# Kernel tuning notes

Measured on AMD Instinct MI355X. Metric: run time of the kernel, lower is better.

The kernel has to match this reference:

```python
import jax, jax.numpy as jnp
import numpy as np

N_NODES = 50000
N_EDGES = 1600000
E_DIM = 128
N_LAYERS = 3
N_GRAPHS = 32


def setup_inputs() -> dict:
    key = jax.random.key(0)
    ks = jax.random.split(key, 12)
    x = jax.random.normal(ks[0], (N_NODES,), dtype=jnp.float32)
    edge_index = jax.random.randint(ks[1], (2, N_EDGES), 0, N_NODES, dtype=jnp.int32)
    batch = jnp.sort(jax.random.randint(ks[2], (N_NODES,), 0, N_GRAPHS, dtype=jnp.int32))
    s_in = 1.0  # fan_in = 1 for the first linear
    s_e = 1.0 / np.sqrt(E_DIM)
    lin_w = jax.random.normal(ks[3], (1, E_DIM), jnp.float32) * s_in
    lin_b = jax.random.normal(ks[4], (E_DIM,), jnp.float32) * 0.01
    gcn_w = jax.random.normal(ks[5], (N_LAYERS, E_DIM, E_DIM), jnp.float32) * s_e
    gcn_b = jax.random.normal(ks[6], (N_LAYERS, E_DIM), jnp.float32) * 0.01
    r1_w = jax.random.normal(ks[7], (E_DIM, E_DIM), jnp.float32) * s_e
    r1_b = jax.random.normal(ks[8], (E_DIM,), jnp.float32) * 0.01
    r2_w = jax.random.normal(ks[9], (E_DIM, 1), jnp.float32) * s_e
    r2_b = jax.random.normal(ks[10], (1,), jnp.float32) * 0.01
    return {"x": x, "edge_index": edge_index, "batch": batch,
            "lin_w": lin_w, "lin_b": lin_b, "gcn_w": gcn_w, "gcn_b": gcn_b,
            "r1_w": r1_w, "r1_b": r1_b, "r2_w": r2_w, "r2_b": r2_b}


def reference(x, edge_index, batch, lin_w, lin_b, gcn_w, gcn_b, r1_w, r1_b, r2_w, r2_b):
    # input embedding: x.view(-1, 1) @ W + b -> [N, E]
    h = x.reshape(-1, 1) @ lin_w + lin_b

    # GCN normalization (add self-loops, symmetric deg^-1/2 norm) — structure is
    # identical across layers, so compute once.
    loops = jnp.arange(N_NODES, dtype=edge_index.dtype)
    src = jnp.concatenate([edge_index[0], loops])
    dst = jnp.concatenate([edge_index[1], loops])
    deg = jax.ops.segment_sum(jnp.ones(src.shape[0], h.dtype), dst, num_segments=N_NODES)
    dinv = jnp.where(deg > 0, jax.lax.rsqrt(deg), 0.0)
    norm = (dinv[src] * dinv[dst])[:, None]  # [E+N, 1]

    # NOTE: original calls x.relu() without assignment -> no activation (faithful).
    for l in range(N_LAYERS):
        h = h @ gcn_w[l]                                        # [N, E]
        h = jax.ops.segment_sum(h[src] * norm, dst, num_segments=N_NODES) + gcn_b[l]

    # global_add_pool over graphs
    pooled = jax.ops.segment_sum(h, batch, num_segments=N_GRAPHS)  # [G, E]
    hr = jnp.tanh(pooled @ r1_w + r1_b)
    return hr @ r2_w + r2_b  # [G, 1]
```

## Files before the change

### kernel.cpp

```cpp
#include <hip/hip_runtime.h>
#include <math.h>

#define NGRAPH 32
#define CAP 10240
#define EPT 16
#define EPB (256 * EPT)
#define BLK 256

__device__ __forceinline__ int block_scan_excl(int v, int tid, int* wsum, int& total) {
    int x = v;
#pragma unroll
    for (int d = 1; d < 64; d <<= 1) {
        int t = __shfl_up(x, d);
        if ((tid & 63) >= d) x += t;
    }
    if ((tid & 63) == 63) wsum[tid >> 6] = x;
    __syncthreads();
    if (tid == 0) {
        int a = 0;
#pragma unroll
        for (int i = 0; i < 4; i++) { int t = wsum[i]; wsum[i] = a; a += t; }
        wsum[4] = a;
    }
    __syncthreads();
    total = wsum[4];
    return x - v + wsum[tid >> 6];
}

__global__ __launch_bounds__(256, 4) void k_part(
        const int* __restrict__ src, const int* __restrict__ dst,
        int* __restrict__ gcursor, unsigned int* __restrict__ packed, int E) {
    __shared__ unsigned int ldsbuf[EPB];
    __shared__ int hist[256], lofs[256], lcur[256], base[256], wsum[5];
    int tid = threadIdx.x;
    int e0 = blockIdx.x * EPB;
    hist[tid] = 0;
    __syncthreads();
    int d_[EPT], s_[EPT];
#pragma unroll
    for (int c = 0; c < EPT / 4; c++) {
        int e = e0 + c * 1024 + (tid << 2);
        if (e + 3 < E) {
            int4 dv = *(const int4*)&dst[e];
            int4 sv = *(const int4*)&src[e];
            d_[4*c+0] = dv.x; d_[4*c+1] = dv.y; d_[4*c+2] = dv.z; d_[4*c+3] = dv.w;
            s_[4*c+0] = sv.x; s_[4*c+1] = sv.y; s_[4*c+2] = sv.z; s_[4*c+3] = sv.w;
            atomicAdd(&hist[dv.x >> 8], 1);
            atomicAdd(&hist[dv.y >> 8], 1);
            atomicAdd(&hist[dv.z >> 8], 1);
            atomicAdd(&hist[dv.w >> 8], 1);
        } else {
#pragma unroll
            for (int k = 0; k < 4; k++) {
                int ee = e + k;
                if (ee < E) {
                    d_[4*c+k] = dst[ee]; s_[4*c+k] = src[ee];
                    atomicAdd(&hist[d_[4*c+k] >> 8], 1);
                } else {
                    d_[4*c+k] = -1;
                }
            }
        }
    }
    __syncthreads();
    int v = hist[tid];
    int total;
    int excl = block_scan_excl(v, tid, wsum, total);
    lofs[tid] = excl;
    lcur[tid] = excl;
    if (v > 0) base[tid] = tid * CAP + atomicAdd(&gcursor[tid], v);
    __syncthreads();
#pragma unroll
    for (int c = 0; c < EPT; c++) {
        int dd = d_[c];
        if (dd >= 0) {
            int bk = dd >> 8;
            int slot = atomicAdd(&lcur[bk], 1);
            ldsbuf[slot] = ((unsigned int)bk << 24) | ((unsigned int)s_[c] << 8)
                         | (unsigned int)(dd & 255);
        }
    }
    __syncthreads();
    for (int i = tid; i < total; i += BLK) {
        unsigned int w = ldsbuf[i];
        int bk = w >> 24;
        packed[base[bk] + (i - lofs[bk])] = w & 0xFFFFFFu;
    }
}

__global__ __launch_bounds__(256) void k_bucket_chain(
        const unsigned int* __restrict__ packed, const int* __restrict__ gcursor,
        const float* __restrict__ x, const int* __restrict__ batch,
        int2* __restrict__ meta, float2* __restrict__ q0,
        float2* __restrict__ q1, float2* __restrict__ q2,
        unsigned short* __restrict__ csr, float* __restrict__ S, int N, int NB,
        const float* __restrict__ lin_w, const float* __restrict__ lin_b,
        const float* __restrict__ gcn_w, const float* __restrict__ gcn_b,
        float* __restrict__ chainv) {
    __shared__ union {
        struct {
            unsigned int buf[CAP];
            __align__(16) unsigned short lcsr[CAP];
            int cnt[256], lcur[256], wsum[5];
            float cs[NGRAPH];
        } b;
        struct { float v4[512]; } c;
    } sm;
    int tid = threadIdx.x;
    int b = blockIdx.x;

    if (b == NB) {
        float* v4 = sm.c.v4;
        int j = tid & 127, gg = tid >> 7;
        if (tid < 128) {
            v4[tid]       = lin_w[tid];
            v4[128 + tid] = lin_b[tid];
            v4[256 + tid] = gcn_b[tid];
            v4[384 + tid] = gcn_b[128 + tid];
        }
        __syncthreads();
        for (int l = 0; l < 3; l++) {
            const float* W = gcn_w + l * 128 * 128;
            float a0 = 0.f, a1 = 0.f;
            for (int k0 = 0; k0 < 128; k0 += 16) {
                float wreg[16];
#pragma unroll
                for (int t = 0; t < 16; t++) wreg[t] = W[(k0 + t) * 128 + j];
#pragma unroll
                for (int t = 0; t < 16; t++) {
                    a0 += v4[gg * 128 + k0 + t] * wreg[t];
                    a1 += v4[(gg + 2) * 128 + k0 + t] * wreg[t];
                }
            }
            __syncthreads();
            v4[gg * 128 + j] = a0;
            bool upd = (gg == 0) ? (l >= 1) : (l >= 2);
            if (upd) v4[(gg + 2) * 128 + j] = a1;
            __syncthreads();
        }
        chainv[tid]       = v4[tid];
        chainv[256 + tid] = v4[256 + tid];
        return;
    }

    int start = b * CAP;
    int len = gcursor[b];
    sm.b.cnt[tid] = 0;
    if (tid < NGRAPH) sm.b.cs[tid] = 0.f;
    __syncthreads();
    for (int e = tid; e < len; e += BLK) {
        unsigned int w = packed[start + e];
        sm.b.buf[e] = w;
        atomicAdd(&sm.b.cnt[w & 255], 1);
    }
    __syncthreads();
    int v = sm.b.cnt[tid];
    int vp = (v + 3) & ~3;
    int total;
    int excl = block_scan_excl(vp, tid, sm.b.wsum, total);
    sm.b.lcur[tid] = excl;
    int node = b * 256 + tid;
    if (node < N) {
        meta[node] = make_int2(start + excl, v);
        float dv = rsqrtf((float)(v + 1));
        q0[node] = make_float2(x[node] * dv, dv);
        atomicAdd(&sm.b.cs[batch[node]], 1.f);
        for (int p = v; p < vp; p++)
            sm.b.lcsr[excl + p] = (unsigned short)N;
    }
    if (b == 0 && tid == 0) {
        q0[N] = make_float2(0.f, 0.f);
        q1[N] = make_float2(0.f, 0.f);
        q2[N] = make_float2(0.f, 0.f);
    }
    __syncthreads();
    for (int e = tid; e < len; e += BLK) {
        unsigned int w = sm.b.buf[e];
        sm.b.lcsr[atomicAdd(&sm.b.lcur[w & 255], 1)] = (unsigned short)(w >> 8);
    }
    if (tid < NGRAPH && sm.b.cs[tid] != 0.f) atomicAdd(&S[tid], sm.b.cs[tid]);
    __syncthreads();
    const uint2* ls = (const uint2*)sm.b.lcsr;
    uint2* gs = (uint2*)&csr[start];
    for (int i = tid; i < (total >> 2); i += BLK) gs[i] = ls[i];
}

__global__ __launch_bounds__(256) void k_hop1(
        const float2* __restrict__ qin, float2* __restrict__ outv,
        const unsigned short* __restrict__ csr,
        const int2* __restrict__ meta, int N) {
    int tid  = threadIdx.x;
    int lane = tid & 7;
    int node = blockIdx.x * 32 + (tid >> 3);
    if (node >= N) return;
    int2 md = meta[node];
    int e = md.x, ne = md.y;
    float sx = 0.0f, su = 0.0f;
    for (int j = 4 * lane; j < ne; j += 32) {
        ushort4 c = *(const ushort4*)&csr[e + j];
        float2 a0 = qin[c.x], a1 = qin[c.y], a2 = qin[c.z], a3 = qin[c.w];
        sx += (a0.x + a1.x) + (a2.x + a3.x);
        su += (a0.y + a1.y) + (a2.y + a3.y);
    }
#pragma unroll
    for (int m = 4; m > 0; m >>= 1) {
        sx += __shfl_xor(sx, m);
        su += __shfl_xor(su, m);
    }
    if (lane == 0) {
        float2 qs = qin[node];
        float dv = rsqrtf((float)(ne + 1));
        float px = dv * (sx + qs.x), pu = dv * (su + qs.y);
        outv[node] = make_float2(px * dv, pu * dv);
    }
}

__global__ __launch_bounds__(256) void k_hop2(
        const float2* __restrict__ qin, float2* __restrict__ outv,
        const unsigned short* __restrict__ csr,
        const int2* __restrict__ meta, const int* __restrict__ batch,
        float* __restrict__ gp1, int N, int NBLK) {
    __shared__ float aS[NGRAPH];
    int tid  = threadIdx.x;
    int lane = tid & 7;
    int node = blockIdx.x * 32 + (tid >> 3);
    if (tid < NGRAPH) aS[tid] = 0.f;
    __syncthreads();
    if (node < N) {
        int2 md = meta[node];
        int e = md.x, ne = md.y;
        float sx = 0.0f, su = 0.0f;
        for (int j = 4 * lane; j < ne; j += 32) {
            ushort4 c = *(const ushort4*)&csr[e + j];
            float2 a0 = qin[c.x], a1 = qin[c.y], a2 = qin[c.z], a3 = qin[c.w];
            sx += (a0.x + a1.x) + (a2.x + a3.x);
            su += (a0.y + a1.y) + (a2.y + a3.y);
        }
#pragma unroll
        for (int m = 4; m > 0; m >>= 1) {
            sx += __shfl_xor(sx, m);
            su += __shfl_xor(su, m);
        }
        if (lane == 0) {
            float2 qs = qin[node];
            float dv = rsqrtf((float)(ne + 1));
            float px = dv * (sx + qs.x), pu = dv * (su + qs.y);
            outv[node] = make_float2(px * dv, pu * dv);
            atomicAdd(&aS[batch[node]], qs.y * sqrtf((float)(ne + 1)));
        }
    }
    __syncthreads();
    if (tid < NGRAPH) gp1[tid * NBLK + blockIdx.x] = aS[tid];
}

__global__ __launch_bounds__(256) void k_hop3(
        const float2* __restrict__ qin,
        const unsigned short* __restrict__ csr,
        const int2* __restrict__ meta, const int* __restrict__ batch,
        float* __restrict__ gp2, float* __restrict__ gp3, float* __restrict__ gp4,
        int N, int NBLK) {
    __shared__ float aS[NGRAPH], aV[NGRAPH], aU[NGRAPH];
    int tid  = threadIdx.x;
    int lane = tid & 7;
    int node = blockIdx.x * 32 + (tid >> 3);
    if (tid < NGRAPH) { aS[tid] = 0.f; aV[tid] = 0.f; aU[tid] = 0.f; }
    __syncthreads();
    if (node < N) {
        int2 md = meta[node];
        int e = md.x, ne = md.y;
        float sx = 0.0f, su = 0.0f;
        for (int j = 4 * lane; j < ne; j += 32) {
            ushort4 c = *(const ushort4*)&csr[e + j];
            float2 a0 = qin[c.x], a1 = qin[c.y], a2 = qin[c.z], a3 = qin[c.w];
            sx += (a0.x + a1.x) + (a2.x + a3.x);
            su += (a0.y + a1.y) + (a2.y + a3.y);
        }
#pragma unroll
        for (int m = 4; m > 0; m >>= 1) {
            sx += __shfl_xor(sx, m);
            su += __shfl_xor(su, m);
        }
        if (lane == 0) {
            float2 qs = qin[node];
            float dv = rsqrtf((float)(ne + 1));
            float px = dv * (sx + qs.x), pu = dv * (su + qs.y);
            int g = batch[node];
            atomicAdd(&aS[g], qs.y * sqrtf((float)(ne + 1)));
            atomicAdd(&aV[g], px);
            atomicAdd(&aU[g], pu);
        }
    }
    __syncthreads();
    if (tid < NGRAPH) {
        int slot = tid * NBLK + blockIdx.x;
        gp2[slot] = aS[tid];
        gp3[slot] = aV[tid];
        gp4[slot] = aU[tid];
    }
}

__global__ __launch_bounds__(256) void k_mlp(
        const float* __restrict__ S, const float* __restrict__ chainv,
        const float* __restrict__ gp1, const float* __restrict__ gp2,
        const float* __restrict__ gp3, const float* __restrict__ gp4,
        const float* __restrict__ gcn_b,
        const float* __restrict__ r1_w, const float* __restrict__ r1_b,
        const float* __restrict__ r2_w, const float* __restrict__ r2_b,
        float* __restrict__ out, int NBLK) {
    __shared__ float pl[128], red[128], r4[256];
    int tid = threadIdx.x;
    int g = blockIdx.x;
    float su1 = 0.f, su2 = 0.f, sv3 = 0.f, su3 = 0.f;
    for (int b = tid; b < NBLK; b += BLK) {
        su1 += gp1[g * NBLK + b];
        su2 += gp2[g * NBLK + b];
        sv3 += gp3[g * NBLK + b];
        su3 += gp4[g * NBLK + b];
    }
#pragma unroll
    for (int m = 32; m > 0; m >>= 1) {
        su1 += __shfl_xor(su1, m);
        su2 += __shfl_xor(su2, m);
        su3 += __shfl_xor(su3, m);
        sv3 += __shfl_xor(sv3, m);
    }
    int wv = tid >> 6;
    if ((tid & 63) == 0) {
        r4[wv] = su1; r4[4 + wv] = su2; r4[8 + wv] = su3; r4[12 + wv] = sv3;
    }
    __syncthreads();
    su1 = r4[0] + r4[1] + r4[2] + r4[3];
    su2 = r4[4] + r4[5] + r4[6] + r4[7];
    su3 = r4[8] + r4[9] + r4[10] + r4[11];
    sv3 = r4[12] + r4[13] + r4[14] + r4[15];
    float cnt = S[g];
    const float* b3 = gcn_b + 2 * 128;
    if (tid < 128)
        pl[tid] = sv3 * chainv[tid] + su3 * chainv[128 + tid] + su2 * chainv[256 + tid]
                + su1 * chainv[384 + tid] + cnt * b3[tid];
    __syncthreads();
    int j = tid & 127, half = tid >> 7;
    float acc = 0.f;
#pragma unroll 8
    for (int kk = 0; kk < 64; kk++) {
        int k = half * 64 + kk;
        acc += pl[k] * r1_w[k * 128 + j];
    }
    r4[half * 128 + j] = acc;
    __syncthreads();
    if (tid < 128) {
        float a = r4[tid] + r4[128 + tid] + r1_b[tid];
        red[tid] = tanhf(a) * r2_w[tid];
    }
    __syncthreads();
    for (int sft = 64; sft > 0; sft >>= 1) {
        if (tid < sft) red[tid] += red[tid + sft];
        __syncthreads();
    }
    if (tid == 0) out[g] = red[0] + r2_b[0];
}

extern "C" void kernel_launch(void* const* d_in, const int* in_sizes, int n_in,
                              void* d_out, int out_size, void* d_ws, size_t ws_size,
                              hipStream_t stream) {
    const float* x     = (const float*)d_in[0];
    const int*   eidx  = (const int*)d_in[1];
    const int*   batch = (const int*)d_in[2];
    const float* lin_w = (const float*)d_in[3];
    const float* lin_b = (const float*)d_in[4];
    const float* gcn_w = (const float*)d_in[5];
    const float* gcn_b = (const float*)d_in[6];
    const float* r1_w  = (const float*)d_in[7];
    const float* r1_b  = (const float*)d_in[8];
    const float* r2_w  = (const float*)d_in[9];
    const float* r2_b  = (const float*)d_in[10];

    const int N = in_sizes[0];
    const int E = in_sizes[1] / 2;
    const int* src = eidx;
    const int* dst = eidx + E;
    const int NB = (N + 255) / 256;
    const int hop_blocks = (N + 31) / 32;

    char* w = (char*)d_ws;
    float2* q0      = (float2*)w; w += (size_t)(N + 2) * 8;
    float2* q1      = (float2*)w; w += (size_t)(N + 2) * 8;
    float2* q2      = (float2*)w; w += (size_t)(N + 2) * 8;
    int2*   meta    = (int2*)w;   w += (size_t)N * 8;
    unsigned int* packed = (unsigned int*)w; w += (size_t)256 * CAP * 4;
    float*  gp1     = (float*)w;  w += (size_t)NGRAPH * hop_blocks * 4;
    float*  gp2     = (float*)w;  w += (size_t)NGRAPH * hop_blocks * 4;
    float*  gp3     = (float*)w;  w += (size_t)NGRAPH * hop_blocks * 4;
    float*  gp4     = (float*)w;  w += (size_t)NGRAPH * hop_blocks * 4;
    int*    gcursor = (int*)w;    w += 256 * 4;
    float*  S       = (float*)w;  w += 64 * 4;
    float*  chainv  = (float*)w;  w += 512 * 4;
    unsigned short* csr = (unsigned short*)w; w += (size_t)256 * CAP * 2 + 256;

    hipMemsetAsync(gcursor, 0, 256 * 4 + 64 * 4, stream);

    const int nchunk = (E + EPB - 1) / EPB;
    k_part<<<nchunk, 256, 0, stream>>>(src, dst, gcursor, packed, E);
    k_bucket_chain<<<NB + 1, 256, 0, stream>>>(packed, gcursor, x, batch, meta,
                                               q0, q1, q2, csr, S, N, NB,
                                               lin_w, lin_b, gcn_w, gcn_b, chainv);

    k_hop1<<<hop_blocks, 256, 0, stream>>>(q0, q1, csr, meta, N);
    k_hop2<<<hop_blocks, 256, 0, stream>>>(q1, q2, csr, meta, batch, gp1, N, hop_blocks);
    k_hop3<<<hop_blocks, 256, 0, stream>>>(q2, csr, meta, batch, gp2, gp3, gp4,
                                           N, hop_blocks);

    k_mlp<<<NGRAPH, 256, 0, stream>>>(S, chainv, gp1, gp2, gp3, gp4, gcn_b,
                                      r1_w, r1_b, r2_w, r2_b, (float*)d_out, hop_blocks);
}
```

Measured before the change: 148.5 us.

## Replace global atomic bucket cursors with per-chunk count and offset tables

The partition kernel now writes each chunk's locally bucket-sorted edges to a contiguous slice of the packed buffer. It records per-bucket counts and offsets in transposed tables, so it no longer needs global atomic cursors or the memset that cleared them. The bucket kernel runs 512-thread blocks, and each thread walks one chunk's segment for its bucket, both to count and to scatter into the local CSR. This removes the scattered global writes and global atomics, but each bucket block now gathers many short, serial, non-coalesced segments instead of one contiguous coalesced range.

```diff
diff --git a/kernel.cpp b/kernel.cpp
--- a/kernel.cpp
+++ b/kernel.cpp
@@ -6,34 +6,17 @@
 #define EPT 16
 #define EPB (256 * EPT)
 #define BLK 256
-
-__device__ __forceinline__ int block_scan_excl(int v, int tid, int* wsum, int& total) {
-    int x = v;
-#pragma unroll
-    for (int d = 1; d < 64; d <<= 1) {
-        int t = __shfl_up(x, d);
-        if ((tid & 63) >= d) x += t;
-    }
-    if ((tid & 63) == 63) wsum[tid >> 6] = x;
-    __syncthreads();
-    if (tid == 0) {
-        int a = 0;
-#pragma unroll
-        for (int i = 0; i < 4; i++) { int t = wsum[i]; wsum[i] = a; a += t; }
-        wsum[4] = a;
-    }
-    __syncthreads();
-    total = wsum[4];
-    return x - v + wsum[tid >> 6];
-}
+#define BBLK 512
 
 __global__ __launch_bounds__(256, 4) void k_part(
         const int* __restrict__ src, const int* __restrict__ dst,
-        int* __restrict__ gcursor, unsigned int* __restrict__ packed, int E) {
+        unsigned int* __restrict__ packed, int* __restrict__ cntsT,
+        int* __restrict__ offsT, int E, int nchunk) {
     __shared__ unsigned int ldsbuf[EPB];
-    __shared__ int hist[256], lofs[256], lcur[256], base[256], wsum[5];
+    __shared__ int hist[256], lcur[256], wsum[5];
     int tid = threadIdx.x;
-    int e0 = blockIdx.x * EPB;
+    int bid = blockIdx.x;
+    int e0 = bid * EPB;
     hist[tid] = 0;
     __syncthreads();
     int d_[EPT], s_[EPT];
@@ -64,42 +47,53 @@
     }
     __syncthreads();
     int v = hist[tid];
-    int total;
-    int excl = block_scan_excl(v, tid, wsum, total);
-    lofs[tid] = excl;
+    int x = v;
+#pragma unroll
+    for (int dshift = 1; dshift < 64; dshift <<= 1) {
+        int t = __shfl_up(x, dshift);
+        if ((tid & 63) >= dshift) x += t;
+    }
+    if ((tid & 63) == 63) wsum[tid >> 6] = x;
+    __syncthreads();
+    if (tid == 0) {
+        int a = 0;
+#pragma unroll
+        for (int i = 0; i < 4; i++) { int t = wsum[i]; wsum[i] = a; a += t; }
+        wsum[4] = a;
+    }
+    __syncthreads();
+    int total = wsum[4];
+    int excl = x - v + wsum[tid >> 6];
     lcur[tid] = excl;
-    if (v > 0) base[tid] = tid * CAP + atomicAdd(&gcursor[tid], v);
+    cntsT[(size_t)tid * nchunk + bid] = v;
+    offsT[(size_t)tid * nchunk + bid] = excl;
     __syncthreads();
 #pragma unroll
     for (int c = 0; c < EPT; c++) {
         int dd = d_[c];
         if (dd >= 0) {
-            int bk = dd >> 8;
-            int slot = atomicAdd(&lcur[bk], 1);
-            ldsbuf[slot] = ((unsigned int)bk << 24) | ((unsigned int)s_[c] << 8)
-                         | (unsigned int)(dd & 255);
-        }
-    }
-    __syncthreads();
-    for (int i = tid; i < total; i += BLK) {
-        unsigned int w = ldsbuf[i];
-        int bk = w >> 24;
-        packed[base[bk] + (i - lofs[bk])] = w & 0xFFFFFFu;
-    }
-}
-
-__global__ __launch_bounds__(256) void k_bucket_chain(
-        const unsigned int* __restrict__ packed, const int* __restrict__ gcursor,
+            int slot = atomicAdd(&lcur[dd >> 8], 1);
+            ldsbuf[slot] = ((unsigned int)s_[c] << 8) | (unsigned int)(dd & 255);
+        }
+    }
+    __syncthreads();
+    for (int i = tid; i < total; i += BLK)
+        packed[e0 + i] = ldsbuf[i];
+}
+
+__global__ __launch_bounds__(512) void k_bucket_chain(
+        const unsigned int* __restrict__ packed, const int* __restrict__ cntsT,
+        const int* __restrict__ offsT,
         const float* __restrict__ x, const int* __restrict__ batch,
         int2* __restrict__ meta, float2* __restrict__ q0,
         float2* __restrict__ q1, float2* __restrict__ q2,
-        unsigned short* __restrict__ csr, float* __restrict__ S, int N, int NB,
+        unsigned short* __restrict__ csr, float* __restrict__ S,
+        int N, int NB, int nchunk,
         const float* __restrict__ lin_w, const float* __restrict__ lin_b,
         const float* __restrict__ gcn_w, const float* __restrict__ gcn_b,
         float* __restrict__ chainv) {
     __shared__ union {
         struct {
-            unsigned int buf[CAP];
             __align__(16) unsigned short lcsr[CAP];
             int cnt[256], lcur[256], wsum[5];
             float cs[NGRAPH];
@@ -110,6 +104,7 @@
     int b = blockIdx.x;
 
     if (b == NB) {
+        if (tid >= 256) return;
         float* v4 = sm.c.v4;
         int j = tid & 127, gg = tid >> 7;
         if (tid < 128) {
@@ -143,25 +138,41 @@
         return;
     }
 
-    int start = b * CAP;
-    int len = gcursor[b];
-    sm.b.cnt[tid] = 0;
+    const int* crow = cntsT + (size_t)b * nchunk;
+    const int* orow = offsT + (size_t)b * nchunk;
+    if (tid < 256) sm.b.cnt[tid] = 0;
     if (tid < NGRAPH) sm.b.cs[tid] = 0.f;
     __syncthreads();
-    for (int e = tid; e < len; e += BLK) {
-        unsigned int w = packed[start + e];
-        sm.b.buf[e] = w;
-        atomicAdd(&sm.b.cnt[w & 255], 1);
-    }
-    __syncthreads();
-    int v = sm.b.cnt[tid];
-    int vp = (v + 3) & ~3;
-    int total;
-    int excl = block_scan_excl(vp, tid, sm.b.wsum, total);
-    sm.b.lcur[tid] = excl;
+    for (int r = tid; r < nchunk; r += BBLK) {
+        int len = crow[r];
+        const unsigned int* p = packed + (size_t)r * EPB + orow[r];
+        for (int k = 0; k < len; k++)
+            atomicAdd(&sm.b.cnt[p[k] & 255], 1);
+    }
+    __syncthreads();
+    int v = 0, vp = 0;
+    if (tid < 256) { v = sm.b.cnt[tid]; vp = (v + 3) & ~3; }
+    int xs = vp;
+#pragma unroll
+    for (int dshift = 1; dshift < 64; dshift <<= 1) {
+        int t = __shfl_up(xs, dshift);
+        if ((tid & 63) >= dshift) xs += t;
+    }
+    if (tid < 256 && (tid & 63) == 63) sm.b.wsum[tid >> 6] = xs;
+    __syncthreads();
+    if (tid == 0) {
+        int a = 0;
+#pragma unroll
+        for (int i = 0; i < 4; i++) { int t = sm.b.wsum[i]; sm.b.wsum[i] = a; a += t; }
+        sm.b.wsum[4] = a;
+    }
+    __syncthreads();
+    int total = sm.b.wsum[4];
+    int excl = (tid < 256) ? (xs - vp + sm.b.wsum[tid >> 6]) : 0;
+    if (tid < 256) sm.b.lcur[tid] = excl;
     int node = b * 256 + tid;
-    if (node < N) {
-        meta[node] = make_int2(start + excl, v);
+    if (tid < 256 && node < N) {
+        meta[node] = make_int2(b * CAP + excl, v);
         float dv = rsqrtf((float)(v + 1));
         q0[node] = make_float2(x[node] * dv, dv);
         atomicAdd(&sm.b.cs[batch[node]], 1.f);
@@ -174,15 +185,19 @@
         q2[N] = make_float2(0.f, 0.f);
     }
     __syncthreads();
-    for (int e = tid; e < len; e += BLK) {
-        unsigned int w = sm.b.buf[e];
-        sm.b.lcsr[atomicAdd(&sm.b.lcur[w & 255], 1)] = (unsigned short)(w >> 8);
+    for (int r = tid; r < nchunk; r += BBLK) {
+        int len = crow[r];
+        const unsigned int* p = packed + (size_t)r * EPB + orow[r];
+        for (int k = 0; k < len; k++) {
+            unsigned int w = p[k];
+            sm.b.lcsr[atomicAdd(&sm.b.lcur[w & 255], 1)] = (unsigned short)(w >> 8);
+        }
     }
     if (tid < NGRAPH && sm.b.cs[tid] != 0.f) atomicAdd(&S[tid], sm.b.cs[tid]);
     __syncthreads();
     const uint2* ls = (const uint2*)sm.b.lcsr;
-    uint2* gs = (uint2*)&csr[start];
-    for (int i = tid; i < (total >> 2); i += BLK) gs[i] = ls[i];
+    uint2* gs = (uint2*)&csr[(size_t)b * CAP];
+    for (int i = tid; i < (total >> 2); i += BBLK) gs[i] = ls[i];
 }
 
 __global__ __launch_bounds__(256) void k_hop1(
@@ -381,29 +396,30 @@
     const int* dst = eidx + E;
     const int NB = (N + 255) / 256;
     const int hop_blocks = (N + 31) / 32;
+    const int nchunk = (E + EPB - 1) / EPB;
 
     char* w = (char*)d_ws;
     float2* q0      = (float2*)w; w += (size_t)(N + 2) * 8;
     float2* q1      = (float2*)w; w += (size_t)(N + 2) * 8;
     float2* q2      = (float2*)w; w += (size_t)(N + 2) * 8;
     int2*   meta    = (int2*)w;   w += (size_t)N * 8;
-    unsigned int* packed = (unsigned int*)w; w += (size_t)256 * CAP * 4;
+    unsigned int* packed = (unsigned int*)w; w += (size_t)nchunk * EPB * 4;
+    int*    cntsT   = (int*)w;    w += (size_t)256 * nchunk * 4;
+    int*    offsT   = (int*)w;    w += (size_t)256 * nchunk * 4;
     float*  gp1     = (float*)w;  w += (size_t)NGRAPH * hop_blocks * 4;
     float*  gp2     = (float*)w;  w += (size_t)NGRAPH * hop_blocks * 4;
     float*  gp3     = (float*)w;  w += (size_t)NGRAPH * hop_blocks * 4;
     float*  gp4     = (float*)w;  w += (size_t)NGRAPH * hop_blocks * 4;
-    int*    gcursor = (int*)w;    w += 256 * 4;
     float*  S       = (float*)w;  w += 64 * 4;
     float*  chainv  = (float*)w;  w += 512 * 4;
-    unsigned short* csr = (unsigned short*)w; w += (size_t)256 * CAP * 2 + 256;
-
-    hipMemsetAsync(gcursor, 0, 256 * 4 + 64 * 4, stream);
-
-    const int nchunk = (E + EPB - 1) / EPB;
-    k_part<<<nchunk, 256, 0, stream>>>(src, dst, gcursor, packed, E);
-    k_bucket_chain<<<NB + 1, 256, 0, stream>>>(packed, gcursor, x, batch, meta,
-                                               q0, q1, q2, csr, S, N, NB,
-                                               lin_w, lin_b, gcn_w, gcn_b, chainv);
+    unsigned short* csr = (unsigned short*)w; w += (size_t)NB * CAP * 2 + 256;
+
+    hipMemsetAsync(S, 0, 64 * 4, stream);
+
+    k_part<<<nchunk, 256, 0, stream>>>(src, dst, packed, cntsT, offsT, E, nchunk);
+    k_bucket_chain<<<NB + 1, BBLK, 0, stream>>>(packed, cntsT, offsT, x, batch, meta,
+                                                q0, q1, q2, csr, S, N, NB, nchunk,
+                                                lin_w, lin_b, gcn_w, gcn_b, chainv);
 
     k_hop1<<<hop_blocks, 256, 0, stream>>>(q0, q1, csr, meta, N);
     k_hop2<<<hop_blocks, 256, 0, stream>>>(q1, q2, csr, meta, batch, gp1, N, hop_blocks);
```

Result: slower. 169.7 us (+14.3%).

## Replace two-level bucket partition with global degree count, scan and atomic scatter CSR

Applied to the files above, without the earlier changes.

The CSR build changes from a two-pass LDS bucketed partition (packed buffer plus per-bucket local sort) to a classic count/scan/scatter. A global degree histogram with atomics is followed by a two-kernel exclusive scan, then per-edge global atomics on per-node cursors place sources directly into the CSR. Per-graph node counts are now computed with binary searches over the sorted batch array in the MLP kernel instead of atomics. This drops the intermediate packed buffer and the LDS sort, but adds two more launches and relies on heavily contended global atomics plus random 2-byte scattered writes.

```diff
diff --git a/kernel.cpp b/kernel.cpp
--- a/kernel.cpp
+++ b/kernel.cpp
@@ -2,9 +2,6 @@
 #include <math.h>
 
 #define NGRAPH 32
-#define CAP 10240
-#define EPT 16
-#define EPB (256 * EPT)
 #define BLK 256
 
 __device__ __forceinline__ int block_scan_excl(int v, int tid, int* wsum, int& total) {
@@ -27,90 +24,82 @@
     return x - v + wsum[tid >> 6];
 }
 
-__global__ __launch_bounds__(256, 4) void k_part(
+__global__ __launch_bounds__(256) void k_count(const int* __restrict__ dst,
+                                               int* __restrict__ deg, int E) {
+    int e = blockIdx.x * 1024 + (threadIdx.x << 2);
+    if (e + 3 < E) {
+        int4 d = *(const int4*)&dst[e];
+        atomicAdd(&deg[d.x], 1);
+        atomicAdd(&deg[d.y], 1);
+        atomicAdd(&deg[d.z], 1);
+        atomicAdd(&deg[d.w], 1);
+    } else {
+#pragma unroll
+        for (int k = 0; k < 4; k++) {
+            int ee = e + k;
+            if (ee < E) atomicAdd(&deg[dst[ee]], 1);
+        }
+    }
+}
+
+__global__ __launch_bounds__(256) void k_scan1(const int* __restrict__ deg,
+                                               int* __restrict__ offsL,
+                                               int* __restrict__ blockTot, int N) {
+    __shared__ int wsum[5];
+    int tid = threadIdx.x, b = blockIdx.x;
+    int node = b * 256 + tid;
+    int dg = (node < N) ? deg[node] : 0;
+    int pad = (dg + 3) & ~3;
+    int total;
+    int excl = block_scan_excl(pad, tid, wsum, total);
+    if (node < N) offsL[node] = excl;
+    if (tid == 0) blockTot[b] = total;
+}
+
+__global__ __launch_bounds__(256) void k_scan2(
+        const int* __restrict__ deg, const int* __restrict__ offsL,
+        const int* __restrict__ blockTot, const float* __restrict__ x,
+        int2* __restrict__ meta, int* __restrict__ cursor,
+        unsigned short* __restrict__ csr,
+        float2* __restrict__ q0, float2* __restrict__ q1, float2* __restrict__ q2,
+        int N, int NBL) {
+    __shared__ int tot[256], wred[4];
+    int tid = threadIdx.x, b = blockIdx.x;
+    tot[tid] = (tid < NBL) ? blockTot[tid] : 0;
+    __syncthreads();
+    int part = (tid < b) ? tot[tid] : 0;
+#pragma unroll
+    for (int m = 32; m > 0; m >>= 1) part += __shfl_xor(part, m);
+    if ((tid & 63) == 0) wred[tid >> 6] = part;
+    __syncthreads();
+    int base = wred[0] + wred[1] + wred[2] + wred[3];
+    int node = b * 256 + tid;
+    if (node < N) {
+        int dg = deg[node];
+        int offs = base + offsL[node];
+        meta[node] = make_int2(offs, dg);
+        cursor[node] = offs;
+        float dv = rsqrtf((float)(dg + 1));
+        q0[node] = make_float2(x[node] * dv, dv);
+        int pad = (dg + 3) & ~3;
+        for (int p = dg; p < pad; p++) csr[offs + p] = (unsigned short)N;
+    }
+    if (b == 0 && tid == 0) {
+        q0[N] = make_float2(0.f, 0.f);
+        q1[N] = make_float2(0.f, 0.f);
+        q2[N] = make_float2(0.f, 0.f);
+    }
+}
+
+__global__ __launch_bounds__(256) void k_scatter_chain(
         const int* __restrict__ src, const int* __restrict__ dst,
-        int* __restrict__ gcursor, unsigned int* __restrict__ packed, int E) {
-    __shared__ unsigned int ldsbuf[EPB];
-    __shared__ int hist[256], lofs[256], lcur[256], base[256], wsum[5];
-    int tid = threadIdx.x;
-    int e0 = blockIdx.x * EPB;
-    hist[tid] = 0;
-    __syncthreads();
-    int d_[EPT], s_[EPT];
-#pragma unroll
-    for (int c = 0; c < EPT / 4; c++) {
-        int e = e0 + c * 1024 + (tid << 2);
-        if (e + 3 < E) {
-            int4 dv = *(const int4*)&dst[e];
-            int4 sv = *(const int4*)&src[e];
-            d_[4*c+0] = dv.x; d_[4*c+1] = dv.y; d_[4*c+2] = dv.z; d_[4*c+3] = dv.w;
-            s_[4*c+0] = sv.x; s_[4*c+1] = sv.y; s_[4*c+2] = sv.z; s_[4*c+3] = sv.w;
-            atomicAdd(&hist[dv.x >> 8], 1);
-            atomicAdd(&hist[dv.y >> 8], 1);
-            atomicAdd(&hist[dv.z >> 8], 1);
-            atomicAdd(&hist[dv.w >> 8], 1);
-        } else {
-#pragma unroll
-            for (int k = 0; k < 4; k++) {
-                int ee = e + k;
-                if (ee < E) {
-                    d_[4*c+k] = dst[ee]; s_[4*c+k] = src[ee];
-                    atomicAdd(&hist[d_[4*c+k] >> 8], 1);
-                } else {
-                    d_[4*c+k] = -1;
-                }
-            }
-        }
-    }
-    __syncthreads();
-    int v = hist[tid];
-    int total;
-    int excl = block_scan_excl(v, tid, wsum, total);
-    lofs[tid] = excl;
-    lcur[tid] = excl;
-    if (v > 0) base[tid] = tid * CAP + atomicAdd(&gcursor[tid], v);
-    __syncthreads();
-#pragma unroll
-    for (int c = 0; c < EPT; c++) {
-        int dd = d_[c];
-        if (dd >= 0) {
-            int bk = dd >> 8;
-            int slot = atomicAdd(&lcur[bk], 1);
-            ldsbuf[slot] = ((unsigned int)bk << 24) | ((unsigned int)s_[c] << 8)
-                         | (unsigned int)(dd & 255);
-        }
-    }
-    __syncthreads();
-    for (int i = tid; i < total; i += BLK) {
-        unsigned int w = ldsbuf[i];
-        int bk = w >> 24;
-        packed[base[bk] + (i - lofs[bk])] = w & 0xFFFFFFu;
-    }
-}
-
-__global__ __launch_bounds__(256) void k_bucket_chain(
-        const unsigned int* __restrict__ packed, const int* __restrict__ gcursor,
-        const float* __restrict__ x, const int* __restrict__ batch,
-        int2* __restrict__ meta, float2* __restrict__ q0,
-        float2* __restrict__ q1, float2* __restrict__ q2,
-        unsigned short* __restrict__ csr, float* __restrict__ S, int N, int NB,
+        int* __restrict__ cursor, unsigned short* __restrict__ csr, int E, int nseg,
         const float* __restrict__ lin_w, const float* __restrict__ lin_b,
         const float* __restrict__ gcn_w, const float* __restrict__ gcn_b,
         float* __restrict__ chainv) {
-    __shared__ union {
-        struct {
-            unsigned int buf[CAP];
-            __align__(16) unsigned short lcsr[CAP];
-            int cnt[256], lcur[256], wsum[5];
-            float cs[NGRAPH];
-        } b;
-        struct { float v4[512]; } c;
-    } sm;
+    __shared__ float v4[512];
     int tid = threadIdx.x;
-    int b = blockIdx.x;
-
-    if (b == NB) {
-        float* v4 = sm.c.v4;
+    if ((int)blockIdx.x == nseg) {
         int j = tid & 127, gg = tid >> 7;
         if (tid < 128) {
             v4[tid]       = lin_w[tid];
@@ -142,47 +131,24 @@
         chainv[256 + tid] = v4[256 + tid];
         return;
     }
-
-    int start = b * CAP;
-    int len = gcursor[b];
-    sm.b.cnt[tid] = 0;
-    if (tid < NGRAPH) sm.b.cs[tid] = 0.f;
-    __syncthreads();
-    for (int e = tid; e < len; e += BLK) {
-        unsigned int w = packed[start + e];
-        sm.b.buf[e] = w;
-        atomicAdd(&sm.b.cnt[w & 255], 1);
-    }
-    __syncthreads();
-    int v = sm.b.cnt[tid];
-    int vp = (v + 3) & ~3;
-    int total;
-    int excl = block_scan_excl(vp, tid, sm.b.wsum, total);
-    sm.b.lcur[tid] = excl;
-    int node = b * 256 + tid;
-    if (node < N) {
-        meta[node] = make_int2(start + excl, v);
-        float dv = rsqrtf((float)(v + 1));
-        q0[node] = make_float2(x[node] * dv, dv);
-        atomicAdd(&sm.b.cs[batch[node]], 1.f);
-        for (int p = v; p < vp; p++)
-            sm.b.lcsr[excl + p] = (unsigned short)N;
-    }
-    if (b == 0 && tid == 0) {
-        q0[N] = make_float2(0.f, 0.f);
-        q1[N] = make_float2(0.f, 0.f);
-        q2[N] = make_float2(0.f, 0.f);
-    }
-    __syncthreads();
-    for (int e = tid; e < len; e += BLK) {
-        unsigned int w = sm.b.buf[e];
-        sm.b.lcsr[atomicAdd(&sm.b.lcur[w & 255], 1)] = (unsigned short)(w >> 8);
-    }
-    if (tid < NGRAPH && sm.b.cs[tid] != 0.f) atomicAdd(&S[tid], sm.b.cs[tid]);
-    __syncthreads();
-    const uint2* ls = (const uint2*)sm.b.lcsr;
-    uint2* gs = (uint2*)&csr[start];
-    for (int i = tid; i < (total >> 2); i += BLK) gs[i] = ls[i];
+    int e = blockIdx.x * 1024 + (tid << 2);
+    if (e + 3 < E) {
+        int4 d = *(const int4*)&dst[e];
+        int4 s = *(const int4*)&src[e];
+        int p0 = atomicAdd(&cursor[d.x], 1); csr[p0] = (unsigned short)s.x;
+        int p1 = atomicAdd(&cursor[d.y], 1); csr[p1] = (unsigned short)s.y;
+        int p2 = atomicAdd(&cursor[d.z], 1); csr[p2] = (unsigned short)s.z;
+        int p3 = atomicAdd(&cursor[d.w], 1); csr[p3] = (unsigned short)s.w;
+    } else {
+#pragma unroll
+        for (int k = 0; k < 4; k++) {
+            int ee = e + k;
+            if (ee < E) {
+                int p = atomicAdd(&cursor[dst[ee]], 1);
+                csr[p] = (unsigned short)src[ee];
+            }
+        }
+    }
 }
 
 __global__ __launch_bounds__(256) void k_hop1(
@@ -300,16 +266,24 @@
 }
 
 __global__ __launch_bounds__(256) void k_mlp(
-        const float* __restrict__ S, const float* __restrict__ chainv,
+        const int* __restrict__ batch, const float* __restrict__ chainv,
         const float* __restrict__ gp1, const float* __restrict__ gp2,
         const float* __restrict__ gp3, const float* __restrict__ gp4,
         const float* __restrict__ gcn_b,
         const float* __restrict__ r1_w, const float* __restrict__ r1_b,
         const float* __restrict__ r2_w, const float* __restrict__ r2_b,
-        float* __restrict__ out, int NBLK) {
+        float* __restrict__ out, int NBLK, int N) {
     __shared__ float pl[128], red[128], r4[256];
+    __shared__ float cntSh;
     int tid = threadIdx.x;
     int g = blockIdx.x;
+    if (tid == 0) {
+        int lo = 0, hi = N;
+        while (lo < hi) { int m = (lo + hi) >> 1; if (batch[m] < g) lo = m + 1; else hi = m; }
+        int lb = lo; lo = 0; hi = N;
+        while (lo < hi) { int m = (lo + hi) >> 1; if (batch[m] < g + 1) lo = m + 1; else hi = m; }
+        cntSh = (float)(lo - lb);
+    }
     float su1 = 0.f, su2 = 0.f, sv3 = 0.f, su3 = 0.f;
     for (int b = tid; b < NBLK; b += BLK) {
         su1 += gp1[g * NBLK + b];
@@ -333,7 +307,7 @@
     su2 = r4[4] + r4[5] + r4[6] + r4[7];
     su3 = r4[8] + r4[9] + r4[10] + r4[11];
     sv3 = r4[12] + r4[13] + r4[14] + r4[15];
-    float cnt = S[g];
+    float cnt = cntSh;
     const float* b3 = gcn_b + 2 * 128;
     if (tid < 128)
         pl[tid] = sv3 * chainv[tid] + su3 * chainv[128 + tid] + su2 * chainv[256 + tid]
@@ -379,37 +353,41 @@
     const int E = in_sizes[1] / 2;
     const int* src = eidx;
     const int* dst = eidx + E;
-    const int NB = (N + 255) / 256;
+    const int NBL = (N + 255) / 256;
     const int hop_blocks = (N + 31) / 32;
+    const int nseg = (E + 1023) / 1024;
 
     char* w = (char*)d_ws;
     float2* q0      = (float2*)w; w += (size_t)(N + 2) * 8;
     float2* q1      = (float2*)w; w += (size_t)(N + 2) * 8;
     float2* q2      = (float2*)w; w += (size_t)(N + 2) * 8;
     int2*   meta    = (int2*)w;   w += (size_t)N * 8;
-    unsigned int* packed = (unsigned int*)w; w += (size_t)256 * CAP * 4;
+    int*    deg     = (int*)w;    w += (size_t)N * 4;
+    int*    offsL   = (int*)w;    w += (size_t)N * 4;
+    int*    cursor  = (int*)w;    w += (size_t)N * 4;
+    int*    blockTot= (int*)w;    w += 256 * 4;
     float*  gp1     = (float*)w;  w += (size_t)NGRAPH * hop_blocks * 4;
     float*  gp2     = (float*)w;  w += (size_t)NGRAPH * hop_blocks * 4;
     float*  gp3     = (float*)w;  w += (size_t)NGRAPH * hop_blocks * 4;
     float*  gp4     = (float*)w;  w += (size_t)NGRAPH * hop_blocks * 4;
-    int*    gcursor = (int*)w;    w += 256 * 4;
-    float*  S       = (float*)w;  w += 64 * 4;
     float*  chainv  = (float*)w;  w += 512 * 4;
-    unsigned short* csr = (unsigned short*)w; w += (size_t)256 * CAP * 2 + 256;
-
-    hipMemsetAsync(gcursor, 0, 256 * 4 + 64 * 4, stream);
-
-    const int nchunk = (E + EPB - 1) / EPB;
-    k_part<<<nchunk, 256, 0, stream>>>(src, dst, gcursor, packed, E);
-    k_bucket_chain<<<NB + 1, 256, 0, stream>>>(packed, gcursor, x, batch, meta,
-                                               q0, q1, q2, csr, S, N, NB,
-                                               lin_w, lin_b, gcn_w, gcn_b, chainv);
+    unsigned short* csr = (unsigned short*)w; w += ((size_t)E + 4 * N) * 2 + 256;
+
+    hipMemsetAsync(deg, 0, (size_t)N * 4, stream);
+
+    k_count<<<nseg, 256, 0, stream>>>(dst, deg, E);
+    k_scan1<<<NBL, 256, 0, stream>>>(deg, offsL, blockTot, N);
+    k_scan2<<<NBL, 256, 0, stream>>>(deg, offsL, blockTot, x, meta, cursor, csr,
+                                     q0, q1, q2, N, NBL);
+    k_scatter_chain<<<nseg + 1, 256, 0, stream>>>(src, dst, cursor, csr, E, nseg,
+                                                  lin_w, lin_b, gcn_w, gcn_b, chainv);
 
     k_hop1<<<hop_blocks, 256, 0, stream>>>(q0, q1, csr, meta, N);
     k_hop2<<<hop_blocks, 256, 0, stream>>>(q1, q2, csr, meta, batch, gp1, N, hop_blocks);
     k_hop3<<<hop_blocks, 256, 0, stream>>>(q2, csr, meta, batch, gp2, gp3, gp4,
                                            N, hop_blocks);
 
-    k_mlp<<<NGRAPH, 256, 0, stream>>>(S, chainv, gp1, gp2, gp3, gp4, gcn_b,
-                                      r1_w, r1_b, r2_w, r2_b, (float*)d_out, hop_blocks);
-}
+    k_mlp<<<NGRAPH, 256, 0, stream>>>(batch, chainv, gp1, gp2, gp3, gp4, gcn_b,
+                                      r1_w, r1_b, r2_w, r2_b, (float*)d_out,
+                                      hop_blocks, N);
+}
```

After: 287.1 us. +93.3%, slower.
